# Optimization experiments

Measured on AMD Instinct MI355X. Metric: run time of the kernel, lower is better.

The kernel has to match this reference:

```python
import jax, jax.numpy as jnp
import numpy as np

# Straight-through binarization: forward hard threshold, backward identity.
# Matches BinarizeTensorThresh / BinarizedLinearFunction / BinaryActivation STE
# semantics from the diffnaps my_layers module (grad_weight = g^T x, i.e. the
# continuous weight receives the gradient of the binary weight unchanged).

def make_ste(thresh):
    @jax.custom_vjp
    def f(x):
        return (x >= thresh).astype(x.dtype)
    def fwd(x):
        return f(x), None
    def bwd(_, g):
        return (g,)
    f.defvjp(fwd, bwd)
    return f

ste_half = make_ste(0.5)  # weight binarization threshold (the 0.5 ctor arg)
ste_one = make_ste(1.0)   # activation fires when (pre-act + bias) >= 1

B, D, H, L = 4096, 5000, 2000, 50  # batch, input_dim(items), hidden_dim(patterns), label_dim
DATA_SPARSITY = 0.05


def setup_inputs() -> dict:
    key = jax.random.key(0)
    k = jax.random.split(key, 5)
    # sparse binary transaction data
    x = (jax.random.uniform(k[0], (B, D)) < DATA_SPARSITY).astype(jnp.float32)
    # continuous encoder weight in [0,1); binarized at 0.5 inside forward
    W_enc = jax.random.uniform(k[1], (H, D), dtype=jnp.float32)
    # small negative encoder bias (BinaPs-style init)
    b_enc = -jnp.abs(jax.random.normal(k[2], (H,), dtype=jnp.float32)) * 0.1
    act0_bias = jnp.zeros((H,), jnp.float32)
    act3_bias = jnp.zeros((D,), jnp.float32)
    # classifier_weight = logit(clip(N(0.1, 0.1), 0.01, 0.99)) as in __init__
    y = jnp.clip(0.1 + 0.1 * jax.random.normal(k[3], (L, H), dtype=jnp.float32), 0.01, 0.99)
    classifier_weight = jnp.log(y / (1.0 - y))
    return {
        "x": x,
        "W_enc": W_enc,
        "b_enc": b_enc,
        "act0_bias": act0_bias,
        "act3_bias": act3_bias,
        "classifier_weight": classifier_weight,
    }


def reference(x, W_enc, b_enc, act0_bias, act3_bias, classifier_weight):
    # fc0_enc: binarized-weight linear with bias
    Wb = ste_half(W_enc)                       # [H, D] in {0,1}
    h = x @ Wb.T + b_enc                       # [B, H]
    # act0: binary activation (threshold 1 on biased pre-activation)
    z = ste_one(h + act0_bias)                 # [B, H]
    # classify: sigmoid-gated classifier head (external_classifier=None / mode 'None')
    final_w = jax.nn.sigmoid(classifier_weight / 0.5)  # [L, H]
    classification = z @ final_w.T             # [B, L]
    # fc3_dec: shares the binarized encoder weight, transposed, no bias
    xd = z @ Wb                                # [B, D]
    output = ste_one(xd + act3_bias)           # [B, D]
    return output, classification, z
```

## Files before the change

kernel.cpp:

```cpp
#include <hip/hip_runtime.h>
#include <stdint.h>

static constexpr int Bn = 4096;
static constexpr int Dn = 5000;
static constexpr int Hn = 2000;
static constexpr int Ln = 50;
static constexpr int XW = 80;
static constexpr int Hpad = 2048;
static constexpr int Dpad = 5120;

typedef int v4i __attribute__((ext_vector_type(4)));
typedef int v16i __attribute__((ext_vector_type(16)));

__device__ __forceinline__ int popc_acc(uint64_t v, int acc) {
  acc = __builtin_popcount((uint32_t)v) + acc;
  acc = __builtin_popcount((uint32_t)(v >> 32)) + acc;
  return acc;
}

__global__ void k_pack_i8(const float* __restrict__ src, uint8_t* __restrict__ dst,
                          int nrows_out, int nrows_valid, int ncols_src) {
  int g = (int)blockIdx.x * 256 + (int)threadIdx.x;
  int row = g / (Dpad / 4);
  int c4 = g - row * (Dpad / 4);
  if (row >= nrows_out) return;
  int col = c4 * 4;
  uchar4 o = make_uchar4(0, 0, 0, 0);
  if (row < nrows_valid && col + 3 < ncols_src) {
    const float4 v = *(const float4*)(src + (size_t)row * ncols_src + col);
    o.x = v.x >= 0.5f; o.y = v.y >= 0.5f; o.z = v.z >= 0.5f; o.w = v.w >= 0.5f;
  }
  *(uchar4*)(dst + (size_t)row * Dpad + col) = o;
}

__global__ __launch_bounds__(256) void k_pack_w_dual(const float* __restrict__ W,
                                                     uint8_t* __restrict__ wi8,
                                                     uint8_t* __restrict__ wtd) {
  int d = (int)blockIdx.x * 256 + (int)threadIdx.x;
  int j0 = (int)blockIdx.y * 64;
  bool dv = d < Dn;
  uint64_t colbits = 0;
  for (int r = 0; r < 64; ++r) {
    int j = j0 + r;
    float v = (j < Hn && dv) ? W[(size_t)j * Dn + d] : 0.0f;
    uint8_t bit = (v >= 0.5f) ? 1 : 0;
    wi8[(size_t)j * Dpad + d] = bit;
    colbits |= ((uint64_t)bit) << r;
  }
  uint8_t* dst = wtd + (size_t)d * Hpad + j0;
#pragma unroll
  for (int q = 0; q < 4; ++q) {
    uint32_t u[4];
#pragma unroll
    for (int s = 0; s < 4; ++s) {
      uint32_t nib = (uint32_t)((colbits >> (q * 16 + s * 4)) & 0xFull);
      u[s] = (nib & 1u) | (((nib >> 1) & 1u) << 8) | (((nib >> 2) & 1u) << 16) |
             (((nib >> 3) & 1u) << 24);
    }
    *(uint4*)(dst + q * 16) = make_uint4(u[0], u[1], u[2], u[3]);
  }
}

__global__ void k_pack_x(const float* __restrict__ x, uint64_t* __restrict__ xb2) {
  int g = (int)((blockIdx.x * blockDim.x + threadIdx.x) >> 6);
  int lane = (int)(threadIdx.x & 63);
  constexpr int nq = XW >> 2;
  int row = g / nq;
  int q = g - row * nq;
  if (row >= Bn) return;
  int w0 = q << 2;
  unsigned long long m[4];
#pragma unroll
  for (int e = 0; e < 4; ++e) {
    int col = ((w0 + e) << 6) + lane;
    float v = (col < Dn) ? x[(size_t)row * Dn + col] : 0.0f;
    m[e] = __ballot(v >= 0.5f);
  }
  if (lane < 4) {
    unsigned long long mv = m[0];
    mv = (lane == 1) ? m[1] : mv;
    mv = (lane == 2) ? m[2] : mv;
    mv = (lane == 3) ? m[3] : mv;
    int w = w0 + lane;
    xb2[((size_t)(w >> 1) * Bn + row) * 2 + (w & 1)] = mv;
  }
}

__global__ void k_pack_w(const float* __restrict__ W, uint64_t* __restrict__ wbT) {
  int g = (int)((blockIdx.x * blockDim.x + threadIdx.x) >> 6);
  int lane = (int)(threadIdx.x & 63);
  constexpr int nq = XW >> 2;
  int row = g / nq;
  int q = g - row * nq;
  if (row >= Hn) return;
  int w0 = q << 2;
  unsigned long long m[4];
#pragma unroll
  for (int e = 0; e < 4; ++e) {
    int col = ((w0 + e) << 6) + lane;
    float v = (col < Dn) ? W[(size_t)row * Dn + col] : 0.0f;
    m[e] = __ballot(v >= 0.5f);
  }
  if (lane < 4) {
    unsigned long long mv = m[0];
    mv = (lane == 1) ? m[1] : mv;
    mv = (lane == 2) ? m[2] : mv;
    mv = (lane == 3) ? m[3] : mv;
    wbT[(size_t)(w0 + lane) * Hpad + row] = mv;
  }
}

__global__ void k_transp(const uint64_t* __restrict__ wbT, uint32_t* __restrict__ wt32) {
  int g = (int)((blockIdx.x * blockDim.x + threadIdx.x) >> 6);
  int lane = (int)(threadIdx.x & 63);
  int w = g % XW;
  int jc = g / XW;
  if (jc >= Hpad / 64) return;
  uint64_t word = wbT[(size_t)w * Hpad + jc * 64 + lane];
  uint64_t mym = 0;
#pragma unroll
  for (int e = 0; e < 64; ++e) {
    unsigned long long m = __ballot((word >> e) & 1ull);
    mym = (lane == e) ? m : mym;
  }
  int d = w * 64 + lane;
  wt32[(size_t)(jc * 2) * Dpad + d] = (uint32_t)mym;
  wt32[(size_t)(jc * 2 + 1) * Dpad + d] = (uint32_t)(mym >> 32);
}

__global__ void k_pack_fwT(const float* __restrict__ cw, float* __restrict__ fwT) {
  int idx = blockIdx.x * blockDim.x + threadIdx.x;
  if (idx >= Hn * 64) return;
  int j = idx >> 6, l = idx & 63;
  float v = 0.0f;
  if (l < Ln) {
    float t = 2.0f * cw[(size_t)l * Hn + j];
    v = 1.0f / (1.0f + expf(-t));
  }
  fwT[idx] = v;
}

__global__ void k_zero(float* __restrict__ p, int n) {
  int i = blockIdx.x * blockDim.x + threadIdx.x;
  if (i < n) p[i] = 0.0f;
}

__global__ __launch_bounds__(256) void k_enc_mfma(
    const uint8_t* __restrict__ A, const uint8_t* __restrict__ B,
    const float* __restrict__ b_enc, const float* __restrict__ act0b,
    float* __restrict__ z_out, uint32_t* __restrict__ zb32,
    uint8_t* __restrict__ zi8) {
  __shared__ uint8_t As[128 * 128];
  __shared__ uint8_t Bs[128 * 128];
  int tid = (int)threadIdx.x;
  int bn = (int)blockIdx.x;
  int bm = (int)blockIdx.y;
  int wv = __builtin_amdgcn_readfirstlane(tid >> 6);
  int lane = tid & 63;
  int wm = wv >> 1, wn = wv & 1;

  v16i acc[2][2];
#pragma unroll
  for (int i = 0; i < 2; ++i)
#pragma unroll
    for (int j = 0; j < 2; ++j) acc[i][j] = (v16i)0;

  int srow = tid >> 3;
  int sq = tid & 7;
  int ldsw = srow * 128 + ((sq ^ (srow & 7)) << 4);
  const uint8_t* ap = A + ((size_t)(bm * 128 + srow)) * Dpad + sq * 16;
  const uint8_t* bp = B + ((size_t)(bn * 128 + srow)) * Dpad + sq * 16;

  int arow = wm * 64 + (lane & 31);
  int brow = wn * 64 + (lane & 31);
  int khalf = lane >> 5;
  int asw = arow & 7;
  int bsw = brow & 7;

#pragma unroll 1
  for (int kt = 0; kt < 40; ++kt) {
    int k0 = kt * 128;
    v4i ra[4], rb[4];
#pragma unroll
    for (int i = 0; i < 4; ++i) {
      ra[i] = *(const v4i*)(ap + k0 + (size_t)i * 32 * Dpad);
      rb[i] = *(const v4i*)(bp + k0 + (size_t)i * 32 * Dpad);
    }
    __syncthreads();
#pragma unroll
    for (int i = 0; i < 4; ++i) {
      *(v4i*)(As + i * 4096 + ldsw) = ra[i];
      *(v4i*)(Bs + i * 4096 + ldsw) = rb[i];
    }
    __syncthreads();
#pragma unroll
    for (int kk = 0; kk < 4; ++kk) {
      int kq = kk * 2 + khalf;
      v4i a0 = *(const v4i*)(As + arow * 128 + ((kq ^ asw) << 4));
      v4i a1 = *(const v4i*)(As + (arow + 32) * 128 + ((kq ^ asw) << 4));
      v4i b0 = *(const v4i*)(Bs + brow * 128 + ((kq ^ bsw) << 4));
      v4i b1 = *(const v4i*)(Bs + (brow + 32) * 128 + ((kq ^ bsw) << 4));
      acc[0][0] = __builtin_amdgcn_mfma_i32_32x32x32_i8(a0, b0, acc[0][0], 0, 0, 0);
      acc[0][1] = __builtin_amdgcn_mfma_i32_32x32x32_i8(a0, b1, acc[0][1], 0, 0, 0);
      acc[1][0] = __builtin_amdgcn_mfma_i32_32x32x32_i8(a1, b0, acc[1][0], 0, 0, 0);
      acc[1][1] = __builtin_amdgcn_mfma_i32_32x32x32_i8(a1, b1, acc[1][1], 0, 0, 0);
    }
  }

  int col0 = bn * 128 + wn * 64 + (lane & 31);
#pragma unroll
  for (int ni = 0; ni < 2; ++ni) {
    int j = col0 + ni * 32;
    int js = (j < Hn) ? j : (Hn - 1);
    float be = b_enc[js];
    float ab = act0b[js];
    bool jv = j < Hn;
    int hw = (bn * 128 + wn * 64 + ni * 32) >> 5;
#pragma unroll
    for (int mi = 0; mi < 2; ++mi) {
      int rbase = bm * 128 + wm * 64 + mi * 32;
#pragma unroll
      for (int r = 0; r < 16; ++r) {
        int rloc = (r & 3) + 8 * (r >> 2) + 4 * (lane >> 5);
        int b = rbase + rloc;
        float h = ((float)acc[mi][ni][r] + be) + ab;
        bool zb = jv && (h >= 1.0f);
        if (jv) {
          z_out[(size_t)b * Hn + j] = zb ? 1.0f : 0.0f;
          if (zi8) zi8[(size_t)b * Hpad + j] = zb ? 1 : 0;
        }
        unsigned long long m = __ballot(zb);
        if (lane == 0) {
          int blo = rbase + (r & 3) + 8 * (r >> 2);
          zb32[(size_t)hw * Bn + blo] = (uint32_t)m;
          zb32[(size_t)hw * Bn + blo + 4] = (uint32_t)(m >> 32);
        }
      }
    }
  }
}

__global__ __launch_bounds__(256) void k_dec_mfma(
    const uint8_t* __restrict__ A,
    const uint8_t* __restrict__ B,
    const float* __restrict__ act3b, float* __restrict__ out) {
  __shared__ uint8_t As[128 * 128];
  __shared__ uint8_t Bs[128 * 128];
  int tid = (int)threadIdx.x;
  int bn = (int)blockIdx.x;
  int bm = (int)blockIdx.y;
  int wv = __builtin_amdgcn_readfirstlane(tid >> 6);
  int lane = tid & 63;
  int wm = wv >> 1, wn = wv & 1;

  v16i acc[2][2];
#pragma unroll
  for (int i = 0; i < 2; ++i)
#pragma unroll
    for (int j = 0; j < 2; ++j) acc[i][j] = (v16i)0;

  int srow = tid >> 3;
  int sq = tid & 7;
  int ldsw = srow * 128 + ((sq ^ (srow & 7)) << 4);
  const uint8_t* ap = A + ((size_t)(bm * 128 + srow)) * Hpad + sq * 16;
  const uint8_t* bp = B + ((size_t)(bn * 128 + srow)) * Hpad + sq * 16;

  int arow = wm * 64 + (lane & 31);
  int brow = wn * 64 + (lane & 31);
  int khalf = lane >> 5;
  int asw = arow & 7;
  int bsw = brow & 7;

#pragma unroll 1
  for (int kt = 0; kt < 16; ++kt) {
    int k0 = kt * 128;
    v4i ra[4], rb[4];
#pragma unroll
    for (int i = 0; i < 4; ++i) {
      ra[i] = *(const v4i*)(ap + k0 + (size_t)i * 32 * Hpad);
      rb[i] = *(const v4i*)(bp + k0 + (size_t)i * 32 * Hpad);
    }
    __syncthreads();
#pragma unroll
    for (int i = 0; i < 4; ++i) {
      *(v4i*)(As + i * 4096 + ldsw) = ra[i];
      *(v4i*)(Bs + i * 4096 + ldsw) = rb[i];
    }
    __syncthreads();
#pragma unroll
    for (int kk = 0; kk < 4; ++kk) {
      int kq = kk * 2 + khalf;
      v4i a0 = *(const v4i*)(As + arow * 128 + ((kq ^ asw) << 4));
      v4i a1 = *(const v4i*)(As + (arow + 32) * 128 + ((kq ^ asw) << 4));
      v4i b0 = *(const v4i*)(Bs + brow * 128 + ((kq ^ bsw) << 4));
      v4i b1 = *(const v4i*)(Bs + (brow + 32) * 128 + ((kq ^ bsw) << 4));
      acc[0][0] = __builtin_amdgcn_mfma_i32_32x32x32_i8(a0, b0, acc[0][0], 0, 0, 0);
      acc[0][1] = __builtin_amdgcn_mfma_i32_32x32x32_i8(a0, b1, acc[0][1], 0, 0, 0);
      acc[1][0] = __builtin_amdgcn_mfma_i32_32x32x32_i8(a1, b0, acc[1][0], 0, 0, 0);
      acc[1][1] = __builtin_amdgcn_mfma_i32_32x32x32_i8(a1, b1, acc[1][1], 0, 0, 0);
    }
  }

  int col0 = bn * 128 + wn * 64 + (lane & 31);
#pragma unroll
  for (int ni = 0; ni < 2; ++ni) {
    int d = col0 + ni * 32;
    int ds = (d < Dn) ? d : (Dn - 1);
    float ab = act3b[ds];
    bool dv = d < Dn;
#pragma unroll
    for (int mi = 0; mi < 2; ++mi) {
      int rbase = bm * 128 + wm * 64 + mi * 32;
#pragma unroll
      for (int r = 0; r < 16; ++r) {
        int rloc = (r & 3) + 8 * (r >> 2) + 4 * (lane >> 5);
        int b = rbase + rloc;
        if (dv) out[(size_t)b * Dn + d] = (((float)acc[mi][ni][r] + ab) >= 1.0f) ? 1.0f : 0.0f;
      }
    }
  }
}

__global__ __launch_bounds__(256) void k_enc_bit(const uint64_t* __restrict__ xb2,
                                                 const uint64_t* __restrict__ wbT,
                                                 const float* __restrict__ b_enc,
                                                 const float* __restrict__ act0b,
                                                 float* __restrict__ z_out,
                                                 uint8_t* __restrict__ zb8) {
  __shared__ uint64_t wl[XW][8];
  int tid = (int)threadIdx.x;
  int jg = (int)blockIdx.x;
  int j0 = jg << 3;
#pragma unroll
  for (int k = 0; k < 3; ++k) {
    int idx = k * 256 + tid;
    if (idx < XW * 8) {
      int w = idx >> 3, j = idx & 7;
      wl[w][j] = wbT[(size_t)w * Hpad + j0 + j];
    }
  }
  __syncthreads();
  int wv = __builtin_amdgcn_readfirstlane(tid >> 6);
  int lane = tid & 63;
  int bg = (int)blockIdx.y * 4 + wv;
  int b0 = (bg << 8) + lane;
  int acc[4][8] = {};
  const uint64_t* xp = xb2 + 2 * (size_t)b0;
#pragma unroll 1
  for (int w2 = 0; w2 < XW / 2; ++w2) {
    ulong2 xx[4];
#pragma unroll
    for (int i = 0; i < 4; ++i)
      xx[i] = *(const ulong2*)(xp + ((size_t)w2 * Bn + i * 64) * 2);
#pragma unroll
    for (int t2 = 0; t2 < 4; ++t2) {
      ulong2 wa = *(ulong2*)&wl[2 * w2][2 * t2];
      ulong2 wb = *(ulong2*)&wl[2 * w2 + 1][2 * t2];
#pragma unroll
      for (int i = 0; i < 4; ++i) {
        acc[i][2 * t2]     = popc_acc(xx[i].x & wa.x, acc[i][2 * t2]);
        acc[i][2 * t2 + 1] = popc_acc(xx[i].x & wa.y, acc[i][2 * t2 + 1]);
        acc[i][2 * t2]     = popc_acc(xx[i].y & wb.x, acc[i][2 * t2]);
        acc[i][2 * t2 + 1] = popc_acc(xx[i].y & wb.y, acc[i][2 * t2 + 1]);
      }
    }
  }
  float be[8], ab[8];
#pragma unroll
  for (int t = 0; t < 8; ++t) {
    int j = j0 + t;
    int js = (j < Hn) ? j : (Hn - 1);
    be[t] = b_enc[js];
    ab[t] = act0b[js];
  }
#pragma unroll
  for (int i = 0; i < 4; ++i) {
    int b = b0 + i * 64;
    uint32_t zbyte = 0;
    float zf[8];
#pragma unroll
    for (int t = 0; t < 8; ++t) {
      int j = j0 + t;
      float h = ((float)acc[i][t] + be[t]) + ab[t];
      bool zb = (j < Hn) && (h >= 1.0f);
      zbyte |= zb ? (1u << t) : 0u;
      zf[t] = zb ? 1.0f : 0.0f;
    }
    zb8[((size_t)(jg >> 2) * Bn + b) * 4 + (jg & 3)] = (uint8_t)zbyte;
    if (j0 < Hn) {
      float* zp = z_out + (size_t)b * Hn + j0;
      *(float4*)zp = make_float4(zf[0], zf[1], zf[2], zf[3]);
      *(float4*)(zp + 4) = make_float4(zf[4], zf[5], zf[6], zf[7]);
    }
  }
}

__global__ __launch_bounds__(256, 6) void k_dec_bit(const uint32_t* __restrict__ zb32,
                                                    const uint32_t* __restrict__ wt32,
                                                    const float* __restrict__ act3b,
                                                    float* __restrict__ out) {
  __shared__ uint32_t tl[64][8];
  int tid = (int)threadIdx.x;
  int dc = (int)blockIdx.x;
  int d0 = dc << 3;
  {
#pragma unroll
    for (int k = 0; k < 2; ++k) {
      int e = k * 256 + tid;
      int hw = e >> 3, dl = e & 7;
      tl[hw][dl] = wt32[(size_t)hw * Dpad + d0 + dl];
    }
  }
  __syncthreads();
  int wv = __builtin_amdgcn_readfirstlane(tid >> 6);
  int lane = tid & 63;
  int bg = (int)blockIdx.y * 4 + wv;
  int b0 = (bg << 8) + lane;
  int acc[4][8] = {};
  const uint32_t* zp = zb32 + b0;
  uint32_t z0, z1, z2, z3, n0, n1, n2, n3;
  uint4 wA, wB, wAn, wBn;
  z0 = zp[0]; z1 = zp[64]; z2 = zp[128]; z3 = zp[192];
  wA = *(const uint4*)&tl[0][0];
  wB = *(const uint4*)&tl[0][4];
#define DEC_MAC()                                          \
  do {                                                     \
    acc[0][0] = __builtin_popcount(z0 & wA.x) + acc[0][0]; \
    acc[0][1] = __builtin_popcount(z0 & wA.y) + acc[0][1]; \
    acc[0][2] = __builtin_popcount(z0 & wA.z) + acc[0][2]; \
    acc[0][3] = __builtin_popcount(z0 & wA.w) + acc[0][3]; \
    acc[0][4] = __builtin_popcount(z0 & wB.x) + acc[0][4]; \
    acc[0][5] = __builtin_popcount(z0 & wB.y) + acc[0][5]; \
    acc[0][6] = __builtin_popcount(z0 & wB.z) + acc[0][6]; \
    acc[0][7] = __builtin_popcount(z0 & wB.w) + acc[0][7]; \
    acc[1][0] = __builtin_popcount(z1 & wA.x) + acc[1][0]; \
    acc[1][1] = __builtin_popcount(z1 & wA.y) + acc[1][1]; \
    acc[1][2] = __builtin_popcount(z1 & wA.z) + acc[1][2]; \
    acc[1][3] = __builtin_popcount(z1 & wA.w) + acc[1][3]; \
    acc[1][4] = __builtin_popcount(z1 & wB.x) + acc[1][4]; \
    acc[1][5] = __builtin_popcount(z1 & wB.y) + acc[1][5]; \
    acc[1][6] = __builtin_popcount(z1 & wB.z) + acc[1][6]; \
    acc[1][7] = __builtin_popcount(z1 & wB.w) + acc[1][7]; \
    acc[2][0] = __builtin_popcount(z2 & wA.x) + acc[2][0]; \
    acc[2][1] = __builtin_popcount(z2 & wA.y) + acc[2][1]; \
    acc[2][2] = __builtin_popcount(z2 & wA.z) + acc[2][2]; \
    acc[2][3] = __builtin_popcount(z2 & wA.w) + acc[2][3]; \
    acc[2][4] = __builtin_popcount(z2 & wB.x) + acc[2][4]; \
    acc[2][5] = __builtin_popcount(z2 & wB.y) + acc[2][5]; \
    acc[2][6] = __builtin_popcount(z2 & wB.z) + acc[2][6]; \
    acc[2][7] = __builtin_popcount(z2 & wB.w) + acc[2][7]; \
    acc[3][0] = __builtin_popcount(z3 & wA.x) + acc[3][0]; \
    acc[3][1] = __builtin_popcount(z3 & wA.y) + acc[3][1]; \
    acc[3][2] = __builtin_popcount(z3 & wA.z) + acc[3][2]; \
    acc[3][3] = __builtin_popcount(z3 & wA.w) + acc[3][3]; \
    acc[3][4] = __builtin_popcount(z3 & wB.x) + acc[3][4]; \
    acc[3][5] = __builtin_popcount(z3 & wB.y) + acc[3][5]; \
    acc[3][6] = __builtin_popcount(z3 & wB.z) + acc[3][6]; \
    acc[3][7] = __builtin_popcount(z3 & wB.w) + acc[3][7]; \
  } while (0)
#pragma unroll 1
  for (int hw = 0; hw < 64; ++hw) {
    int hn = (hw < 63) ? hw + 1 : hw;
    const uint32_t* zq = zp + (size_t)hn * Bn;
    n0 = zq[0]; n1 = zq[64]; n2 = zq[128]; n3 = zq[192];
    wAn = *(const uint4*)&tl[hn][0];
    wBn = *(const uint4*)&tl[hn][4];
    DEC_MAC();
    z0 = n0; z1 = n1; z2 = n2; z3 = n3;
    wA = wAn; wB = wBn;
  }
#undef DEC_MAC
  float ab[8];
#pragma unroll
  for (int t = 0; t < 8; ++t) {
    int d = d0 + t;
    int ds = (d < Dn) ? d : (Dn - 1);
    ab[t] = act3b[ds];
  }
  if (d0 < Dn) {
#pragma unroll
    for (int i = 0; i < 4; ++i) {
      int b = b0 + i * 64;
      float of[8];
#pragma unroll
      for (int t = 0; t < 8; ++t)
        of[t] = (((float)acc[i][t] + ab[t]) >= 1.0f) ? 1.0f : 0.0f;
      float* op = out + (size_t)b * Dn + d0;
      *(float4*)op = make_float4(of[0], of[1], of[2], of[3]);
      *(float4*)(op + 4) = make_float4(of[4], of[5], of[6], of[7]);
    }
  }
}

__global__ __launch_bounds__(256) void k_cls_i8(const uint8_t* __restrict__ zi8,
                                                const float* __restrict__ fwT,
                                                float* __restrict__ cls) {
  __shared__ float zT[64][132];
  __shared__ float fwL[64][64];
  int tid = (int)threadIdx.x;
  int bb0 = (int)blockIdx.x * 128;
  int jsp = (int)blockIdx.y;
  int tx = tid & 15, ty = tid >> 4;
  float acc[8][4] = {};
  for (int tile = 0; tile < 4; ++tile) {
    int jt0 = jsp * 256 + tile * 64;
    __syncthreads();
#pragma unroll
    for (int k = 0; k < 8; ++k) {
      int idx = k * 256 + tid;
      int r = idx >> 4, c4 = idx & 15;
      int j = jt0 + c4 * 4;
      uchar4 v = make_uchar4(0, 0, 0, 0);
      if (j < Hn) v = *(const uchar4*)(zi8 + (size_t)(bb0 + r) * Hpad + j);
      zT[c4 * 4 + 0][r] = (float)v.x;
      zT[c4 * 4 + 1][r] = (float)v.y;
      zT[c4 * 4 + 2][r] = (float)v.z;
      zT[c4 * 4 + 3][r] = (float)v.w;
    }
#pragma unroll
    for (int k = 0; k < 4; ++k) {
      int idx = k * 256 + tid;
      int jj = idx >> 4, c4 = idx & 15;
      int j = jt0 + jj;
      float4 v = make_float4(0.f, 0.f, 0.f, 0.f);
      if (j < Hn) v = *(const float4*)(fwT + (size_t)j * 64 + c4 * 4);
      *(float4*)&fwL[jj][c4 * 4] = v;
    }
    __syncthreads();
#pragma unroll 4
    for (int jj = 0; jj < 64; ++jj) {
      float4 fv = *(float4*)&fwL[jj][tx * 4];
      float4 za = *(float4*)&zT[jj][ty * 8];
      float4 zb = *(float4*)&zT[jj][ty * 8 + 4];
      float zz[8] = {za.x, za.y, za.z, za.w, zb.x, zb.y, zb.z, zb.w};
      float ff[4] = {fv.x, fv.y, fv.z, fv.w};
#pragma unroll
      for (int i = 0; i < 8; ++i)
#pragma unroll
        for (int l = 0; l < 4; ++l) acc[i][l] += zz[i] * ff[l];
    }
  }
#pragma unroll
  for (int i = 0; i < 8; ++i) {
    int b = bb0 + ty * 8 + i;
#pragma unroll
    for (int l = 0; l < 4; ++l) {
      int L = tx * 4 + l;
      if (L < Ln) atomicAdd(&cls[(size_t)b * Ln + L], acc[i][l]);
    }
  }
}

__global__ __launch_bounds__(256) void k_cls_f32(const float* __restrict__ z,
                                                 const float* __restrict__ fwT,
                                                 float* __restrict__ cls) {
  __shared__ float zT[64][132];
  __shared__ float fwL[64][64];
  int tid = (int)threadIdx.x;
  int bb0 = (int)blockIdx.x * 128;
  int jsp = (int)blockIdx.y;
  int tx = tid & 15, ty = tid >> 4;
  float acc[8][4] = {};
  for (int tile = 0; tile < 4; ++tile) {
    int jt0 = jsp * 256 + tile * 64;
    __syncthreads();
#pragma unroll
    for (int k = 0; k < 8; ++k) {
      int idx = k * 256 + tid;
      int r = idx >> 4, c4 = idx & 15;
      int j = jt0 + c4 * 4;
      float4 v = make_float4(0.f, 0.f, 0.f, 0.f);
      if (j < Hn) v = *(const float4*)(z + (size_t)(bb0 + r) * Hn + j);
      zT[c4 * 4 + 0][r] = v.x;
      zT[c4 * 4 + 1][r] = v.y;
      zT[c4 * 4 + 2][r] = v.z;
      zT[c4 * 4 + 3][r] = v.w;
    }
#pragma unroll
    for (int k = 0; k < 4; ++k) {
      int idx = k * 256 + tid;
      int jj = idx >> 4, c4 = idx & 15;
      int j = jt0 + jj;
      float4 v = make_float4(0.f, 0.f, 0.f, 0.f);
      if (j < Hn) v = *(const float4*)(fwT + (size_t)j * 64 + c4 * 4);
      *(float4*)&fwL[jj][c4 * 4] = v;
    }
    __syncthreads();
#pragma unroll 4
    for (int jj = 0; jj < 64; ++jj) {
      float4 fv = *(float4*)&fwL[jj][tx * 4];
      float4 za = *(float4*)&zT[jj][ty * 8];
      float4 zb = *(float4*)&zT[jj][ty * 8 + 4];
      float zz[8] = {za.x, za.y, za.z, za.w, zb.x, zb.y, zb.z, zb.w};
      float ff[4] = {fv.x, fv.y, fv.z, fv.w};
#pragma unroll
      for (int i = 0; i < 8; ++i)
#pragma unroll
        for (int l = 0; l < 4; ++l) acc[i][l] += zz[i] * ff[l];
    }
  }
#pragma unroll
  for (int i = 0; i < 8; ++i) {
    int b = bb0 + ty * 8 + i;
#pragma unroll
    for (int l = 0; l < 4; ++l) {
      int L = tx * 4 + l;
      if (L < Ln) atomicAdd(&cls[(size_t)b * Ln + L], acc[i][l]);
    }
  }
}

extern "C" void kernel_launch(void* const* d_in, const int* in_sizes, int n_in,
                              void* d_out, int out_size, void* d_ws, size_t ws_size,
                              hipStream_t stream) {
  const float* x     = (const float*)d_in[0];
  const float* W     = (const float*)d_in[1];
  const float* b_enc = (const float*)d_in[2];
  const float* act0b = (const float*)d_in[3];
  const float* act3b = (const float*)d_in[4];
  const float* cw    = (const float*)d_in[5];

  float* out0 = (float*)d_out;
  float* cls  = out0 + (size_t)Bn * Dn;
  float* zout = cls + (size_t)Bn * Ln;

  char* p = (char*)d_ws;
  uint32_t* zb32 = (uint32_t*)p; p += (size_t)64 * Bn * 4;
  float*    fwT  = (float*)p;    p += (size_t)Hn * 64 * 4;
  size_t common = (size_t)(p - (char*)d_ws);

  size_t sz_xi8 = (size_t)Bn * Dpad;
  size_t sz_wi8 = (size_t)Hpad * Dpad;
  size_t sz_zi8 = (size_t)Bn * Hpad;
  size_t sz_wtd = (size_t)Dpad * Hpad;
  size_t sz_wbT = (size_t)XW * Hpad * 8;
  size_t sz_wt32 = (size_t)64 * Dpad * 4;
  size_t full_need = common + sz_xi8 + sz_wi8 + sz_zi8 + sz_wtd;
  size_t mid_need  = common + sz_wbT + sz_wt32 + sz_xi8 + sz_wi8;

  k_pack_fwT<<<(Hn * 64 + 255) / 256, 256, 0, stream>>>(cw, fwT);
  k_zero<<<(Bn * Ln + 255) / 256, 256, 0, stream>>>(cls, Bn * Ln);

  if (ws_size >= full_need) {
    uint8_t* xi8 = (uint8_t*)p;
    uint8_t* wi8 = xi8 + sz_xi8;
    uint8_t* zi8 = wi8 + sz_wi8;
    uint8_t* wtd = zi8 + sz_zi8;
    k_pack_i8<<<(Bn * (Dpad / 4) + 255) / 256, 256, 0, stream>>>(x, xi8, Bn, Bn, Dn);
    dim3 gwd(Dpad / 256, Hpad / 64);
    k_pack_w_dual<<<gwd, 256, 0, stream>>>(W, wi8, wtd);
    dim3 ge(Hpad / 128, Bn / 128);
    k_enc_mfma<<<ge, 256, 0, stream>>>(xi8, wi8, b_enc, act0b, zout, zb32, zi8);
    dim3 g3(32, 8);
    k_cls_i8<<<g3, 256, 0, stream>>>(zi8, fwT, cls);
    dim3 gd(Dpad / 128, Bn / 128);
    k_dec_mfma<<<gd, 256, 0, stream>>>(zi8, wtd, act3b, out0);
  } else if (ws_size >= mid_need) {
    uint64_t* wbT  = (uint64_t*)p;
    uint32_t* wt32 = (uint32_t*)(p + sz_wbT);
    uint8_t*  xi8  = (uint8_t*)(p + sz_wbT + sz_wt32);
    uint8_t*  wi8  = xi8 + sz_xi8;
    {
      long long waves = (long long)Hn * (XW / 4);
      k_pack_w<<<(int)((waves * 64 + 255) / 256), 256, 0, stream>>>(W, wbT);
    }
    {
      long long waves = (long long)(Hpad / 64) * XW;
      k_transp<<<(int)((waves * 64 + 255) / 256), 256, 0, stream>>>(wbT, wt32);
    }
    k_pack_i8<<<(Bn * (Dpad / 4) + 255) / 256, 256, 0, stream>>>(x, xi8, Bn, Bn, Dn);
    k_pack_i8<<<(Hpad * (Dpad / 4) + 255) / 256, 256, 0, stream>>>(W, wi8, Hpad, Hn, Dn);
    dim3 ge(Hpad / 128, Bn / 128);
    k_enc_mfma<<<ge, 256, 0, stream>>>(xi8, wi8, b_enc, act0b, zout, zb32, (uint8_t*)nullptr);
    dim3 g3(32, 8);
    k_cls_f32<<<g3, 256, 0, stream>>>(zout, fwT, cls);
    dim3 g2(640, 4);
    k_dec_bit<<<g2, 256, 0, stream>>>(zb32, wt32, act3b, out0);
  } else {
    uint64_t* wbT  = (uint64_t*)p;
    uint32_t* wt32 = (uint32_t*)(p + sz_wbT);
    uint64_t* xb2  = (uint64_t*)(p + sz_wbT + sz_wt32);
    {
      long long waves = (long long)Hn * (XW / 4);
      k_pack_w<<<(int)((waves * 64 + 255) / 256), 256, 0, stream>>>(W, wbT);
    }
    {
      long long waves = (long long)(Hpad / 64) * XW;
      k_transp<<<(int)((waves * 64 + 255) / 256), 256, 0, stream>>>(wbT, wt32);
    }
    {
      long long waves = (long long)Bn * (XW / 4);
      k_pack_x<<<(int)((waves * 64 + 255) / 256), 256, 0, stream>>>(x, xb2);
    }
    dim3 g1(256, 4);
    k_enc_bit<<<g1, 256, 0, stream>>>(xb2, wbT, b_enc, act0b, zout, (uint8_t*)zb32);
    dim3 g3(32, 8);
    k_cls_f32<<<g3, 256, 0, stream>>>(zout, fwT, cls);
    dim3 g2(640, 4);
    k_dec_bit<<<g2, 256, 0, stream>>>(zb32, wt32, act3b, out0);
  }
}
```

Before: 238.2 us.

## Use direct global-to-LDS loads in int8 MFMA GEMMs and skip unused bitmask writes

Replaces the register-staged global→LDS tile copy in the encoder and decoder int8 MFMA kernels with the global_load_lds builtin, when the compiler provides it. Each wave writes its 8-row slices straight into LDS, keeping the same XOR swizzle, which removes VGPR staging and the separate ds_write instructions. In the full-workspace path the encoder no longer computes ballots or stores the zb32 bitmask, since only the mid path reads it. The copy is still not double-buffered, so load latency stays exposed between the barriers, and correctness depends on the builtin's per-lane LDS placement matching the swizzle.

```diff
diff --git a/kernel.cpp b/kernel.cpp
--- a/kernel.cpp
+++ b/kernel.cpp
@@ -11,6 +11,20 @@
 
 typedef int v4i __attribute__((ext_vector_type(4)));
 typedef int v16i __attribute__((ext_vector_type(16)));
+
+#if defined(__has_builtin)
+#if __has_builtin(__builtin_amdgcn_global_load_lds)
+#define HAVE_GLOAD_LDS 1
+#endif
+#endif
+
+#ifdef HAVE_GLOAD_LDS
+__device__ __forceinline__ void gload16(const uint8_t* g, uint8_t* l) {
+  __builtin_amdgcn_global_load_lds(
+      (const __attribute__((address_space(1))) uint32_t*)g,
+      (__attribute__((address_space(3))) uint32_t*)l, 16, 0, 0);
+}
+#endif
 
 __device__ __forceinline__ int popc_acc(uint64_t v, int acc) {
   acc = __builtin_popcount((uint32_t)v) + acc;
@@ -165,11 +179,28 @@
 #pragma unroll
     for (int j = 0; j < 2; ++j) acc[i][j] = (v16i)0;
 
+#ifdef HAVE_GLOAD_LDS
+  int srow8 = lane >> 3;
+  int scol = (((lane & 7) ^ srow8) << 4);
+  const uint8_t* aSrc[4];
+  const uint8_t* bSrc[4];
+  uint8_t* aDst[4];
+  uint8_t* bDst[4];
+#pragma unroll
+  for (int i = 0; i < 4; ++i) {
+    int r = i * 32 + wv * 8 + srow8;
+    aSrc[i] = A + (size_t)(bm * 128 + r) * Dpad + scol;
+    bSrc[i] = B + (size_t)(bn * 128 + r) * Dpad + scol;
+    aDst[i] = As + (i * 32 + wv * 8) * 128;
+    bDst[i] = Bs + (i * 32 + wv * 8) * 128;
+  }
+#else
   int srow = tid >> 3;
   int sq = tid & 7;
   int ldsw = srow * 128 + ((sq ^ (srow & 7)) << 4);
   const uint8_t* ap = A + ((size_t)(bm * 128 + srow)) * Dpad + sq * 16;
   const uint8_t* bp = B + ((size_t)(bn * 128 + srow)) * Dpad + sq * 16;
+#endif
 
   int arow = wm * 64 + (lane & 31);
   int brow = wn * 64 + (lane & 31);
@@ -180,6 +211,15 @@
 #pragma unroll 1
   for (int kt = 0; kt < 40; ++kt) {
     int k0 = kt * 128;
+#ifdef HAVE_GLOAD_LDS
+    __syncthreads();
+#pragma unroll
+    for (int i = 0; i < 4; ++i) {
+      gload16(aSrc[i] + k0, aDst[i]);
+      gload16(bSrc[i] + k0, bDst[i]);
+    }
+    __syncthreads();
+#else
     v4i ra[4], rb[4];
 #pragma unroll
     for (int i = 0; i < 4; ++i) {
@@ -193,6 +233,7 @@
       *(v4i*)(Bs + i * 4096 + ldsw) = rb[i];
     }
     __syncthreads();
+#endif
 #pragma unroll
     for (int kk = 0; kk < 4; ++kk) {
       int kq = kk * 2 + khalf;
@@ -229,11 +270,13 @@
           z_out[(size_t)b * Hn + j] = zb ? 1.0f : 0.0f;
           if (zi8) zi8[(size_t)b * Hpad + j] = zb ? 1 : 0;
         }
-        unsigned long long m = __ballot(zb);
-        if (lane == 0) {
-          int blo = rbase + (r & 3) + 8 * (r >> 2);
-          zb32[(size_t)hw * Bn + blo] = (uint32_t)m;
-          zb32[(size_t)hw * Bn + blo + 4] = (uint32_t)(m >> 32);
+        if (zb32) {
+          unsigned long long m = __ballot(zb);
+          if (lane == 0) {
+            int blo = rbase + (r & 3) + 8 * (r >> 2);
+            zb32[(size_t)hw * Bn + blo] = (uint32_t)m;
+            zb32[(size_t)hw * Bn + blo + 4] = (uint32_t)(m >> 32);
+          }
         }
       }
     }
@@ -259,11 +302,28 @@
 #pragma unroll
     for (int j = 0; j < 2; ++j) acc[i][j] = (v16i)0;
 
+#ifdef HAVE_GLOAD_LDS
+  int srow8 = lane >> 3;
+  int scol = (((lane & 7) ^ srow8) << 4);
+  const uint8_t* aSrc[4];
+  const uint8_t* bSrc[4];
+  uint8_t* aDst[4];
+  uint8_t* bDst[4];
+#pragma unroll
+  for (int i = 0; i < 4; ++i) {
+    int r = i * 32 + wv * 8 + srow8;
+    aSrc[i] = A + (size_t)(bm * 128 + r) * Hpad + scol;
+    bSrc[i] = B + (size_t)(bn * 128 + r) * Hpad + scol;
+    aDst[i] = As + (i * 32 + wv * 8) * 128;
+    bDst[i] = Bs + (i * 32 + wv * 8) * 128;
+  }
+#else
   int srow = tid >> 3;
   int sq = tid & 7;
   int ldsw = srow * 128 + ((sq ^ (srow & 7)) << 4);
   const uint8_t* ap = A + ((size_t)(bm * 128 + srow)) * Hpad + sq * 16;
   const uint8_t* bp = B + ((size_t)(bn * 128 + srow)) * Hpad + sq * 16;
+#endif
 
   int arow = wm * 64 + (lane & 31);
   int brow = wn * 64 + (lane & 31);
@@ -274,6 +334,15 @@
 #pragma unroll 1
   for (int kt = 0; kt < 16; ++kt) {
     int k0 = kt * 128;
+#ifdef HAVE_GLOAD_LDS
+    __syncthreads();
+#pragma unroll
+    for (int i = 0; i < 4; ++i) {
+      gload16(aSrc[i] + k0, aDst[i]);
+      gload16(bSrc[i] + k0, bDst[i]);
+    }
+    __syncthreads();
+#else
     v4i ra[4], rb[4];
 #pragma unroll
     for (int i = 0; i < 4; ++i) {
@@ -287,6 +356,7 @@
       *(v4i*)(Bs + i * 4096 + ldsw) = rb[i];
     }
     __syncthreads();
+#endif
 #pragma unroll
     for (int kk = 0; kk < 4; ++kk) {
       int kq = kk * 2 + khalf;
@@ -650,7 +720,8 @@
     dim3 gwd(Dpad / 256, Hpad / 64);
     k_pack_w_dual<<<gwd, 256, 0, stream>>>(W, wi8, wtd);
     dim3 ge(Hpad / 128, Bn / 128);
-    k_enc_mfma<<<ge, 256, 0, stream>>>(xi8, wi8, b_enc, act0b, zout, zb32, zi8);
+    k_enc_mfma<<<ge, 256, 0, stream>>>(xi8, wi8, b_enc, act0b, zout,
+                                       (uint32_t*)nullptr, zi8);
     dim3 g3(32, 8);
     k_cls_i8<<<g3, 256, 0, stream>>>(zi8, fwT, cls);
     dim3 gd(Dpad / 128, Bn / 128);
@@ -671,7 +742,8 @@
     k_pack_i8<<<(Bn * (Dpad / 4) + 255) / 256, 256, 0, stream>>>(x, xi8, Bn, Bn, Dn);
     k_pack_i8<<<(Hpad * (Dpad / 4) + 255) / 256, 256, 0, stream>>>(W, wi8, Hpad, Hn, Dn);
     dim3 ge(Hpad / 128, Bn / 128);
-    k_enc_mfma<<<ge, 256, 0, stream>>>(xi8, wi8, b_enc, act0b, zout, zb32, (uint8_t*)nullptr);
+    k_enc_mfma<<<ge, 256, 0, stream>>>(xi8, wi8, b_enc, act0b, zout, zb32,
+                                       (uint8_t*)nullptr);
     dim3 g3(32, 8);
     k_cls_f32<<<g3, 256, 0, stream>>>(zout, fwT, cls);
     dim3 g2(640, 4);
```

Result: no change. 235.9 us (-1.0%).

## Double-buffer int8 MFMA GEMMs with direct global-to-LDS loads

Applied to the files above, without the earlier changes.

Both int8 MFMA GEMM kernels now share a macro that uses global_load_lds to copy 64-wide K tiles straight into double-buffered LDS. The next tile is prefetched while MFMAs run on the current one, and each K step needs one barrier instead of two with register staging. The encoder epilogue drops the bit-packed zb32 ballot stores and always writes zi8, and the mid-workspace fallback path is removed. This adds reliance on the builtin being available and on the new swizzle layout being correct, and it shrinks K per tile, which doubles the number of loop iterations.

```diff
diff --git a/kernel.cpp b/kernel.cpp
--- a/kernel.cpp
+++ b/kernel.cpp
@@ -11,6 +11,20 @@
 
 typedef int v4i __attribute__((ext_vector_type(4)));
 typedef int v16i __attribute__((ext_vector_type(16)));
+
+#if defined(__has_builtin)
+#if __has_builtin(__builtin_amdgcn_global_load_lds)
+#define HAVE_GLOAD_LDS 1
+#endif
+#endif
+
+#ifdef HAVE_GLOAD_LDS
+__device__ __forceinline__ void gload16(const uint8_t* g, uint8_t* l) {
+  __builtin_amdgcn_global_load_lds(
+      (const __attribute__((address_space(1))) uint32_t*)g,
+      (__attribute__((address_space(3))) uint32_t*)l, 16, 0, 0);
+}
+#endif
 
 __device__ __forceinline__ int popc_acc(uint64_t v, int acc) {
   acc = __builtin_popcount((uint32_t)v) + acc;
@@ -145,13 +159,111 @@
   if (i < n) p[i] = 0.0f;
 }
 
+
+#ifdef HAVE_GLOAD_LDS
+#define GEMM_PIPE(LDK, NT, Abase, Bbase)                                        \
+  int srow_l = lane >> 2;                                           \
+  int scol = (((lane & 3) ^ ((lane >> 3) & 3)) << 4);                          \
+  const uint8_t* aSrc[2];                                                      \
+  const uint8_t* bSrc[2];                                                      \
+  uint8_t* asd[2][2];                                                          \
+  uint8_t* bsd[2][2];                                                          \
+  _Pragma("unroll") for (int i = 0; i < 2; ++i) {                              \
+    int rbaseS = wv * 32 + i * 16;                                             \
+    aSrc[i] = (Abase) + (size_t)(bm * 128 + rbaseS + srow_l) * (LDK) + scol;   \
+    bSrc[i] = (Bbase) + (size_t)(bn * 128 + rbaseS + srow_l) * (LDK) + scol;   \
+    asd[0][i] = As + rbaseS * 64;                                              \
+    asd[1][i] = As + 8192 + rbaseS * 64;                                       \
+    bsd[0][i] = Bs + rbaseS * 64;                                              \
+    bsd[1][i] = Bs + 8192 + rbaseS * 64;                                       \
+  }                                                                            \
+  int arow = wm * 64 + (lane & 31);                                            \
+  int brow = wn * 64 + (lane & 31);                                            \
+  int khalf = lane >> 5;                                                       \
+  int asl = (arow >> 1) & 3;                                                   \
+  int bsl = (brow >> 1) & 3;                                                   \
+                                                                 \
+  _Pragma("unroll") for (int i = 0; i < 2; ++i) {                              \
+    gload16(aSrc[i], asd[0][i]);                                               \
+    gload16(bSrc[i], bsd[0][i]);                                               \
+  }                                                                            \
+  __syncthreads();                                                             \
+  _Pragma("unroll 1") for (int t = 0; t < (NT); ++t) {                         \
+    int cur = t & 1;                                                           \
+    if (t + 1 < (NT)) {                                                        \
+      size_t koff = (size_t)(t + 1) * 64;                                      \
+      _Pragma("unroll") for (int i = 0; i < 2; ++i) {                          \
+        gload16(aSrc[i] + koff, asd[cur ^ 1][i]);                              \
+        gload16(bSrc[i] + koff, bsd[cur ^ 1][i]);                              \
+      }                                                                        \
+    }                                                                          \
+    const uint8_t* Ab = As + cur * 8192;                                       \
+    const uint8_t* Bb = Bs + cur * 8192;                                       \
+    _Pragma("unroll") for (int kk = 0; kk < 2; ++kk) {                         \
+      int kq = kk * 2 + khalf;                                                 \
+      v4i a0 = *(const v4i*)(Ab + arow * 64 + ((kq ^ asl) << 4));              \
+      v4i a1 = *(const v4i*)(Ab + (arow + 32) * 64 + ((kq ^ asl) << 4));       \
+      v4i b0 = *(const v4i*)(Bb + brow * 64 + ((kq ^ bsl) << 4));              \
+      v4i b1 = *(const v4i*)(Bb + (brow + 32) * 64 + ((kq ^ bsl) << 4));       \
+      acc[0][0] = __builtin_amdgcn_mfma_i32_32x32x32_i8(a0, b0, acc[0][0], 0, 0, 0); \
+      acc[0][1] = __builtin_amdgcn_mfma_i32_32x32x32_i8(a0, b1, acc[0][1], 0, 0, 0); \
+      acc[1][0] = __builtin_amdgcn_mfma_i32_32x32x32_i8(a1, b0, acc[1][0], 0, 0, 0); \
+      acc[1][1] = __builtin_amdgcn_mfma_i32_32x32x32_i8(a1, b1, acc[1][1], 0, 0, 0); \
+    }                                                                          \
+    __syncthreads();                                                           \
+  }
+#else
+#define GEMM_PIPE(LDK, NT, Abase, Bbase)                                       \
+  int srow_l = tid >> 2;                                            \
+  int sq = tid & 3;                                                            \
+  const uint8_t* ap0 = (Abase) + (size_t)(bm * 128 + srow_l) * (LDK) + sq * 16;\
+  const uint8_t* ap1 = ap0 + (size_t)64 * (LDK);                               \
+  const uint8_t* bp0 = (Bbase) + (size_t)(bn * 128 + srow_l) * (LDK) + sq * 16;\
+  const uint8_t* bp1 = bp0 + (size_t)64 * (LDK);                               \
+  int lw0 = srow_l * 64 + ((sq ^ ((srow_l >> 1) & 3)) << 4);                   \
+  int lw1 = (64 + srow_l) * 64 + ((sq ^ (((64 + srow_l) >> 1) & 3)) << 4);     \
+  int arow = wm * 64 + (lane & 31);                                            \
+  int brow = wn * 64 + (lane & 31);                                            \
+  int khalf = lane >> 5;                                                       \
+  int asl = (arow >> 1) & 3;                                                   \
+  int bsl = (brow >> 1) & 3;                                                   \
+  _Pragma("unroll 1") for (int t = 0; t < (NT); ++t) {                         \
+    size_t koff = (size_t)t * 64;                                              \
+    v4i ra0 = *(const v4i*)(ap0 + koff);                                       \
+    v4i ra1 = *(const v4i*)(ap1 + koff);                                       \
+    v4i rb0 = *(const v4i*)(bp0 + koff);                                       \
+    v4i rb1 = *(const v4i*)(bp1 + koff);                                       \
+    __syncthreads();                                                           \
+    *(v4i*)(As + lw0) = ra0;                                                   \
+    *(v4i*)(As + lw1) = ra1;                                                   \
+    *(v4i*)(Bs + lw0) = rb0;                                                   \
+    *(v4i*)(Bs + lw1) = rb1;                                                   \
+    __syncthreads();                                                           \
+    _Pragma("unroll") for (int kk = 0; kk < 2; ++kk) {                         \
+      int kq = kk * 2 + khalf;                                                 \
+      v4i a0 = *(const v4i*)(As + arow * 64 + ((kq ^ asl) << 4));              \
+      v4i a1 = *(const v4i*)(As + (arow + 32) * 64 + ((kq ^ asl) << 4));       \
+      v4i b0 = *(const v4i*)(Bs + brow * 64 + ((kq ^ bsl) << 4));              \
+      v4i b1 = *(const v4i*)(Bs + (brow + 32) * 64 + ((kq ^ bsl) << 4));       \
+      acc[0][0] = __builtin_amdgcn_mfma_i32_32x32x32_i8(a0, b0, acc[0][0], 0, 0, 0); \
+      acc[0][1] = __builtin_amdgcn_mfma_i32_32x32x32_i8(a0, b1, acc[0][1], 0, 0, 0); \
+      acc[1][0] = __builtin_amdgcn_mfma_i32_32x32x32_i8(a1, b0, acc[1][0], 0, 0, 0); \
+      acc[1][1] = __builtin_amdgcn_mfma_i32_32x32x32_i8(a1, b1, acc[1][1], 0, 0, 0); \
+    }                                                                          \
+  }
+#endif
+
 __global__ __launch_bounds__(256) void k_enc_mfma(
     const uint8_t* __restrict__ A, const uint8_t* __restrict__ B,
     const float* __restrict__ b_enc, const float* __restrict__ act0b,
-    float* __restrict__ z_out, uint32_t* __restrict__ zb32,
-    uint8_t* __restrict__ zi8) {
-  __shared__ uint8_t As[128 * 128];
-  __shared__ uint8_t Bs[128 * 128];
+    float* __restrict__ z_out, uint8_t* __restrict__ zi8) {
+#ifdef HAVE_GLOAD_LDS
+  __shared__ uint8_t As[2 * 128 * 64];
+  __shared__ uint8_t Bs[2 * 128 * 64];
+#else
+  __shared__ uint8_t As[128 * 64];
+  __shared__ uint8_t Bs[128 * 64];
+#endif
   int tid = (int)threadIdx.x;
   int bn = (int)blockIdx.x;
   int bm = (int)blockIdx.y;
@@ -165,47 +277,7 @@
 #pragma unroll
     for (int j = 0; j < 2; ++j) acc[i][j] = (v16i)0;
 
-  int srow = tid >> 3;
-  int sq = tid & 7;
-  int ldsw = srow * 128 + ((sq ^ (srow & 7)) << 4);
-  const uint8_t* ap = A + ((size_t)(bm * 128 + srow)) * Dpad + sq * 16;
-  const uint8_t* bp = B + ((size_t)(bn * 128 + srow)) * Dpad + sq * 16;
-
-  int arow = wm * 64 + (lane & 31);
-  int brow = wn * 64 + (lane & 31);
-  int khalf = lane >> 5;
-  int asw = arow & 7;
-  int bsw = brow & 7;
-
-#pragma unroll 1
-  for (int kt = 0; kt < 40; ++kt) {
-    int k0 = kt * 128;
-    v4i ra[4], rb[4];
-#pragma unroll
-    for (int i = 0; i < 4; ++i) {
-      ra[i] = *(const v4i*)(ap + k0 + (size_t)i * 32 * Dpad);
-      rb[i] = *(const v4i*)(bp + k0 + (size_t)i * 32 * Dpad);
-    }
-    __syncthreads();
-#pragma unroll
-    for (int i = 0; i < 4; ++i) {
-      *(v4i*)(As + i * 4096 + ldsw) = ra[i];
-      *(v4i*)(Bs + i * 4096 + ldsw) = rb[i];
-    }
-    __syncthreads();
-#pragma unroll
-    for (int kk = 0; kk < 4; ++kk) {
-      int kq = kk * 2 + khalf;
-      v4i a0 = *(const v4i*)(As + arow * 128 + ((kq ^ asw) << 4));
-      v4i a1 = *(const v4i*)(As + (arow + 32) * 128 + ((kq ^ asw) << 4));
-      v4i b0 = *(const v4i*)(Bs + brow * 128 + ((kq ^ bsw) << 4));
-      v4i b1 = *(const v4i*)(Bs + (brow + 32) * 128 + ((kq ^ bsw) << 4));
-      acc[0][0] = __builtin_amdgcn_mfma_i32_32x32x32_i8(a0, b0, acc[0][0], 0, 0, 0);
-      acc[0][1] = __builtin_amdgcn_mfma_i32_32x32x32_i8(a0, b1, acc[0][1], 0, 0, 0);
-      acc[1][0] = __builtin_amdgcn_mfma_i32_32x32x32_i8(a1, b0, acc[1][0], 0, 0, 0);
-      acc[1][1] = __builtin_amdgcn_mfma_i32_32x32x32_i8(a1, b1, acc[1][1], 0, 0, 0);
-    }
-  }
+  GEMM_PIPE(Dpad, Dpad / 64, A, B)
 
   int col0 = bn * 128 + wn * 64 + (lane & 31);
 #pragma unroll
@@ -215,7 +287,6 @@
     float be = b_enc[js];
     float ab = act0b[js];
     bool jv = j < Hn;
-    int hw = (bn * 128 + wn * 64 + ni * 32) >> 5;
 #pragma unroll
     for (int mi = 0; mi < 2; ++mi) {
       int rbase = bm * 128 + wm * 64 + mi * 32;
@@ -227,13 +298,7 @@
         bool zb = jv && (h >= 1.0f);
         if (jv) {
           z_out[(size_t)b * Hn + j] = zb ? 1.0f : 0.0f;
-          if (zi8) zi8[(size_t)b * Hpad + j] = zb ? 1 : 0;
-        }
-        unsigned long long m = __ballot(zb);
-        if (lane == 0) {
-          int blo = rbase + (r & 3) + 8 * (r >> 2);
-          zb32[(size_t)hw * Bn + blo] = (uint32_t)m;
-          zb32[(size_t)hw * Bn + blo + 4] = (uint32_t)(m >> 32);
+          zi8[(size_t)b * Hpad + j] = zb ? 1 : 0;
         }
       }
     }
@@ -244,8 +309,13 @@
     const uint8_t* __restrict__ A,
     const uint8_t* __restrict__ B,
     const float* __restrict__ act3b, float* __restrict__ out) {
-  __shared__ uint8_t As[128 * 128];
-  __shared__ uint8_t Bs[128 * 128];
+#ifdef HAVE_GLOAD_LDS
+  __shared__ uint8_t As[2 * 128 * 64];
+  __shared__ uint8_t Bs[2 * 128 * 64];
+#else
+  __shared__ uint8_t As[128 * 64];
+  __shared__ uint8_t Bs[128 * 64];
+#endif
   int tid = (int)threadIdx.x;
   int bn = (int)blockIdx.x;
   int bm = (int)blockIdx.y;
@@ -259,47 +329,7 @@
 #pragma unroll
     for (int j = 0; j < 2; ++j) acc[i][j] = (v16i)0;
 
-  int srow = tid >> 3;
-  int sq = tid & 7;
-  int ldsw = srow * 128 + ((sq ^ (srow & 7)) << 4);
-  const uint8_t* ap = A + ((size_t)(bm * 128 + srow)) * Hpad + sq * 16;
-  const uint8_t* bp = B + ((size_t)(bn * 128 + srow)) * Hpad + sq * 16;
-
-  int arow = wm * 64 + (lane & 31);
-  int brow = wn * 64 + (lane & 31);
-  int khalf = lane >> 5;
-  int asw = arow & 7;
-  int bsw = brow & 7;
-
-#pragma unroll 1
-  for (int kt = 0; kt < 16; ++kt) {
-    int k0 = kt * 128;
-    v4i ra[4], rb[4];
-#pragma unroll
-    for (int i = 0; i < 4; ++i) {
-      ra[i] = *(const v4i*)(ap + k0 + (size_t)i * 32 * Hpad);
-      rb[i] = *(const v4i*)(bp + k0 + (size_t)i * 32 * Hpad);
-    }
-    __syncthreads();
-#pragma unroll
-    for (int i = 0; i < 4; ++i) {
-      *(v4i*)(As + i * 4096 + ldsw) = ra[i];
-      *(v4i*)(Bs + i * 4096 + ldsw) = rb[i];
-    }
-    __syncthreads();
-#pragma unroll
-    for (int kk = 0; kk < 4; ++kk) {
-      int kq = kk * 2 + khalf;
-      v4i a0 = *(const v4i*)(As + arow * 128 + ((kq ^ asw) << 4));
-      v4i a1 = *(const v4i*)(As + (arow + 32) * 128 + ((kq ^ asw) << 4));
-      v4i b0 = *(const v4i*)(Bs + brow * 128 + ((kq ^ bsw) << 4));
-      v4i b1 = *(const v4i*)(Bs + (brow + 32) * 128 + ((kq ^ bsw) << 4));
-      acc[0][0] = __builtin_amdgcn_mfma_i32_32x32x32_i8(a0, b0, acc[0][0], 0, 0, 0);
-      acc[0][1] = __builtin_amdgcn_mfma_i32_32x32x32_i8(a0, b1, acc[0][1], 0, 0, 0);
-      acc[1][0] = __builtin_amdgcn_mfma_i32_32x32x32_i8(a1, b0, acc[1][0], 0, 0, 0);
-      acc[1][1] = __builtin_amdgcn_mfma_i32_32x32x32_i8(a1, b1, acc[1][1], 0, 0, 0);
-    }
-  }
+  GEMM_PIPE(Hpad, Hpad / 64, A, B)
 
   int col0 = bn * 128 + wn * 64 + (lane & 31);
 #pragma unroll
@@ -636,7 +666,6 @@
   size_t sz_wbT = (size_t)XW * Hpad * 8;
   size_t sz_wt32 = (size_t)64 * Dpad * 4;
   size_t full_need = common + sz_xi8 + sz_wi8 + sz_zi8 + sz_wtd;
-  size_t mid_need  = common + sz_wbT + sz_wt32 + sz_xi8 + sz_wi8;
 
   k_pack_fwT<<<(Hn * 64 + 255) / 256, 256, 0, stream>>>(cw, fwT);
   k_zero<<<(Bn * Ln + 255) / 256, 256, 0, stream>>>(cls, Bn * Ln);
@@ -650,32 +679,11 @@
     dim3 gwd(Dpad / 256, Hpad / 64);
     k_pack_w_dual<<<gwd, 256, 0, stream>>>(W, wi8, wtd);
     dim3 ge(Hpad / 128, Bn / 128);
-    k_enc_mfma<<<ge, 256, 0, stream>>>(xi8, wi8, b_enc, act0b, zout, zb32, zi8);
+    k_enc_mfma<<<ge, 256, 0, stream>>>(xi8, wi8, b_enc, act0b, zout, zi8);
     dim3 g3(32, 8);
     k_cls_i8<<<g3, 256, 0, stream>>>(zi8, fwT, cls);
     dim3 gd(Dpad / 128, Bn / 128);
     k_dec_mfma<<<gd, 256, 0, stream>>>(zi8, wtd, act3b, out0);
-  } else if (ws_size >= mid_need) {
-    uint64_t* wbT  = (uint64_t*)p;
-    uint32_t* wt32 = (uint32_t*)(p + sz_wbT);
-    uint8_t*  xi8  = (uint8_t*)(p + sz_wbT + sz_wt32);
-    uint8_t*  wi8  = xi8 + sz_xi8;
-    {
-      long long waves = (long long)Hn * (XW / 4);
-      k_pack_w<<<(int)((waves * 64 + 255) / 256), 256, 0, stream>>>(W, wbT);
-    }
-    {
-      long long waves = (long long)(Hpad / 64) * XW;
-      k_transp<<<(int)((waves * 64 + 255) / 256), 256, 0, stream>>>(wbT, wt32);
-    }
-    k_pack_i8<<<(Bn * (Dpad / 4) + 255) / 256, 256, 0, stream>>>(x, xi8, Bn, Bn, Dn);
-    k_pack_i8<<<(Hpad * (Dpad / 4) + 255) / 256, 256, 0, stream>>>(W, wi8, Hpad, Hn, Dn);
-    dim3 ge(Hpad / 128, Bn / 128);
-    k_enc_mfma<<<ge, 256, 0, stream>>>(xi8, wi8, b_enc, act0b, zout, zb32, (uint8_t*)nullptr);
-    dim3 g3(32, 8);
-    k_cls_f32<<<g3, 256, 0, stream>>>(zout, fwT, cls);
-    dim3 g2(640, 4);
-    k_dec_bit<<<g2, 256, 0, stream>>>(zb32, wt32, act3b, out0);
   } else {
     uint64_t* wbT  = (uint64_t*)p;
     uint32_t* wt32 = (uint32_t*)(p + sz_wbT);
```

Result: slower. 246.0 us (+3.3%).
